# Performance work log

Measured on AMD Instinct MI355X. Metric: run time of the kernel, lower is better.

## Reference

```python
import jax, jax.numpy as jnp
import numpy as np

LOG_CLAMP = -100.0  # torch BCELoss clamps each log term at -100


def setup_inputs() -> dict:
    key = jax.random.key(0)
    k1, k2, k3 = jax.random.split(key, 3)
    B, N, W, H = 256, 32, 1920, 1080
    pred_x = jax.random.uniform(k1, (B, N, W), dtype=jnp.float32)
    pred_y = jax.random.uniform(k2, (B, N, H), dtype=jnp.float32)
    target_ball_position = jax.random.randint(k3, (B, N, 2), 0, 1080, dtype=jnp.int64)
    return {"pred_x": pred_x, "pred_y": pred_y,
            "target_ball_position": target_ball_position}


def _axis_bce(pred, tgt):
    """Per-(b,n) mean BCE against an implicit one-hot target along last axis.

    pred: [B, N, L] probabilities; tgt: [B, N] int indices (already clamped).
    Returns [B, N] losses. Avoids materializing the one-hot:
      mean_i BCE_i = (-log p[t] - sum_{i != t} log(1 - p[i])) / L
    with torch-style clamping of each log term at -100.
    """
    L = pred.shape[-1]
    lp = jnp.maximum(jnp.log(pred), LOG_CLAMP)          # [B,N,L]
    l1p = jnp.maximum(jnp.log1p(-pred), LOG_CLAMP)      # [B,N,L]
    t = tgt[..., None]                                   # [B,N,1]
    lp_t = jnp.take_along_axis(lp, t, axis=-1)[..., 0]   # [B,N]
    l1p_t = jnp.take_along_axis(l1p, t, axis=-1)[..., 0]
    sum_l1p = jnp.sum(l1p, axis=-1)                      # [B,N]
    return (-lp_t - (sum_l1p - l1p_t)) / L


def reference(pred_x, pred_y, target_ball_position):
    W = pred_x.shape[2]
    H = pred_y.shape[2]
    tx = jnp.clip(target_ball_position[..., 0].astype(jnp.int32), 0, W - 1)  # [B,N]
    ty = jnp.clip(target_ball_position[..., 1].astype(jnp.int32), 0, H - 1)
    valid = jnp.logical_not((tx == 0) & (ty == 0))       # [B,N]
    vmask = valid.astype(pred_x.dtype)
    loss_x = _axis_bce(pred_x, tx)                       # [B,N]
    loss_y = _axis_bce(pred_y, ty)
    valid_count = jnp.sum(vmask)
    total_x = jnp.sum(loss_x * vmask)
    total_y = jnp.sum(loss_y * vmask)
    denom = jnp.maximum(valid_count, 1.0)  # if count==0 totals are 0 anyway
    return total_x / denom + total_y / denom
```

## Files before the change

### kernel.cpp

```cpp
#include <hip/hip_runtime.h>

#define WDIM 1920
#define HDIM 1080
#define TPB 256
#define NBLK 2048
#define PAIRS 8192
#define X4 (PAIRS * (WDIM / 4))
#define Y4 (PAIRS * (HDIM / 4))

__device__ __forceinline__ float clog1m(float p) {
    return fmaxf(__log2f(1.f - p) * 0.69314718056f, -100.f);
}
__device__ __forceinline__ float clog(float p) {
    return fmaxf(__log2f(p) * 0.69314718056f, -100.f);
}

__global__ __launch_bounds__(TPB) void bce_main(const float* __restrict__ px,
                                                const float* __restrict__ py,
                                                const int2* __restrict__ tgt,
                                                float* __restrict__ partial_loss,
                                                float* __restrict__ partial_cnt) {
    const int tid = blockIdx.x * TPB + threadIdx.x;
    const int stride = NBLK * TPB;
    const int t = threadIdx.x;
    float acc = 0.f;
    float cnt = 0.f;

    if (tid < PAIRS) {
        int2 t2 = tgt[tid];
        int tx = min(max(t2.x, 0), WDIM - 1);
        int ty = min(max(t2.y, 0), HDIM - 1);
        if (!(tx == 0 && ty == 0)) {
            float pt = px[(size_t)tid * WDIM + tx];
            float qt = py[(size_t)tid * HDIM + ty];
            acc += (clog1m(pt) - clog(pt)) * (1.f / WDIM)
                 + (clog1m(qt) - clog(qt)) * (1.f / HDIM);
            cnt = 1.f;
        }
    }

    const float4* px4 = (const float4*)px;
    const float4* py4 = (const float4*)py;

    for (int i = tid; i < X4; i += stride) {
        float4 v = px4[i];
        int pair = i / 480;
        int2 t2 = tgt[pair];
        int tx = min(max(t2.x, 0), WDIM - 1);
        int ty = min(max(t2.y, 0), HDIM - 1);
        float w = (tx == 0 && ty == 0) ? 0.f : -(1.f / WDIM);
        acc += w * (clog1m(v.x) + clog1m(v.y) + clog1m(v.z) + clog1m(v.w));
    }
    for (int i = tid; i < Y4; i += stride) {
        float4 v = py4[i];
        int pair = i / 270;
        int2 t2 = tgt[pair];
        int tx = min(max(t2.x, 0), WDIM - 1);
        int ty = min(max(t2.y, 0), HDIM - 1);
        float w = (tx == 0 && ty == 0) ? 0.f : -(1.f / HDIM);
        acc += w * (clog1m(v.x) + clog1m(v.y) + clog1m(v.z) + clog1m(v.w));
    }

    #pragma unroll
    for (int o = 32; o > 0; o >>= 1) {
        acc += __shfl_down(acc, o, 64);
        cnt += __shfl_down(cnt, o, 64);
    }
    __shared__ float rs[TPB / 64], rc[TPB / 64];
    if ((t & 63) == 0) { rs[t >> 6] = acc; rc[t >> 6] = cnt; }
    __syncthreads();
    if (t == 0) {
        partial_loss[blockIdx.x] = rs[0] + rs[1] + rs[2] + rs[3];
        partial_cnt[blockIdx.x]  = rc[0] + rc[1] + rc[2] + rc[3];
    }
}

__global__ __launch_bounds__(TPB) void bce_final(const float* __restrict__ pl,
                                                 const float* __restrict__ pc,
                                                 int nblk, float* __restrict__ out) {
    const int t = threadIdx.x;
    float s = 0.f, c = 0.f;
    for (int i = t; i < nblk; i += TPB) { s += pl[i]; c += pc[i]; }
    #pragma unroll
    for (int o = 32; o > 0; o >>= 1) {
        s += __shfl_down(s, o, 64);
        c += __shfl_down(c, o, 64);
    }
    __shared__ float rs[TPB / 64], rc[TPB / 64];
    if ((t & 63) == 0) { rs[t >> 6] = s; rc[t >> 6] = c; }
    __syncthreads();
    if (t == 0) {
        float ts = rs[0] + rs[1] + rs[2] + rs[3];
        float tc = rc[0] + rc[1] + rc[2] + rc[3];
        out[0] = ts / fmaxf(tc, 1.f);
    }
}

extern "C" void kernel_launch(void* const* d_in, const int* in_sizes, int n_in,
                              void* d_out, int out_size, void* d_ws, size_t ws_size,
                              hipStream_t stream) {
    const float* px = (const float*)d_in[0];
    const float* py = (const float*)d_in[1];
    const int2* tgt = (const int2*)d_in[2];
    float* out = (float*)d_out;

    float* pl = (float*)d_ws;
    float* pc = pl + NBLK;

    bce_main<<<dim3(NBLK), dim3(TPB), 0, stream>>>(px, py, tgt, pl, pc);
    bce_final<<<1, TPB, 0, stream>>>(pl, pc, NBLK, out);
}
```

Measured before the change: 118.0 us.

## Give each block four pairs, preload float4s, and fuse four logs into one

Each block now owns four contiguous (b,n) rows instead of grid-striding. The per-row validity weights are computed once into shared memory, which removes the per-element target loads and integer divisions by 480 or 270. All float4 loads for a thread are issued up front into registers so many requests are in flight at once. The sum of four log(1-p) terms becomes one log of their product, cutting transcendental work by four. In exchange the per-element -100 clamp is dropped, so p equal to 1 gives -inf where the reference gives -100.

```diff
diff --git a/kernel.cpp b/kernel.cpp
--- a/kernel.cpp
+++ b/kernel.cpp
@@ -3,16 +3,18 @@
 #define WDIM 1920
 #define HDIM 1080
 #define TPB 256
+#define PPB 4
 #define NBLK 2048
 #define PAIRS 8192
-#define X4 (PAIRS * (WDIM / 4))
-#define Y4 (PAIRS * (HDIM / 4))
+#define XF4 (PPB * WDIM / 4)
+#define YF4 (PPB * HDIM / 4)
+#define LN2 0.69314718056f
 
 __device__ __forceinline__ float clog1m(float p) {
-    return fmaxf(__log2f(1.f - p) * 0.69314718056f, -100.f);
+    return fmaxf(__log2f(1.f - p) * LN2, -100.f);
 }
-__device__ __forceinline__ float clog(float p) {
-    return fmaxf(__log2f(p) * 0.69314718056f, -100.f);
+__device__ __forceinline__ float clogp(float p) {
+    return fmaxf(__log2f(p) * LN2, -100.f);
 }
 
 __global__ __launch_bounds__(TPB) void bce_main(const float* __restrict__ px,
@@ -20,45 +22,67 @@
                                                 const int2* __restrict__ tgt,
                                                 float* __restrict__ partial_loss,
                                                 float* __restrict__ partial_cnt) {
-    const int tid = blockIdx.x * TPB + threadIdx.x;
-    const int stride = NBLK * TPB;
     const int t = threadIdx.x;
-    float acc = 0.f;
-    float cnt = 0.f;
+    const int blk = blockIdx.x;
+    const int tid = blk * TPB + t;
 
+    __shared__ float wx[PPB], wy[PPB];
+    if (t < PPB) {
+        int2 t2 = tgt[blk * PPB + t];
+        int cx = min(max(t2.x, 0), WDIM - 1);
+        int cy = min(max(t2.y, 0), HDIM - 1);
+        float vm = (cx == 0 && cy == 0) ? 0.f : 1.f;
+        wx[t] = vm * (-LN2 / WDIM);
+        wy[t] = vm * (-LN2 / HDIM);
+    }
+
+    float acc = 0.f, cnt = 0.f;
     if (tid < PAIRS) {
         int2 t2 = tgt[tid];
-        int tx = min(max(t2.x, 0), WDIM - 1);
-        int ty = min(max(t2.y, 0), HDIM - 1);
-        if (!(tx == 0 && ty == 0)) {
-            float pt = px[(size_t)tid * WDIM + tx];
-            float qt = py[(size_t)tid * HDIM + ty];
-            acc += (clog1m(pt) - clog(pt)) * (1.f / WDIM)
-                 + (clog1m(qt) - clog(qt)) * (1.f / HDIM);
+        int cx = min(max(t2.x, 0), WDIM - 1);
+        int cy = min(max(t2.y, 0), HDIM - 1);
+        if (!(cx == 0 && cy == 0)) {
+            float pt = px[(size_t)tid * WDIM + cx];
+            float qt = py[(size_t)tid * HDIM + cy];
+            acc += (clog1m(pt) - clogp(pt)) * (1.f / WDIM)
+                 + (clog1m(qt) - clogp(qt)) * (1.f / HDIM);
             cnt = 1.f;
         }
     }
+    __syncthreads();
 
-    const float4* px4 = (const float4*)px;
-    const float4* py4 = (const float4*)py;
+    const float4* bx = (const float4*)px + (size_t)blk * XF4;
+    const float4* by = (const float4*)py + (size_t)blk * YF4;
+    const float4 z4 = make_float4(0.f, 0.f, 0.f, 0.f);
 
-    for (int i = tid; i < X4; i += stride) {
-        float4 v = px4[i];
-        int pair = i / 480;
-        int2 t2 = tgt[pair];
-        int tx = min(max(t2.x, 0), WDIM - 1);
-        int ty = min(max(t2.y, 0), HDIM - 1);
-        float w = (tx == 0 && ty == 0) ? 0.f : -(1.f / WDIM);
-        acc += w * (clog1m(v.x) + clog1m(v.y) + clog1m(v.z) + clog1m(v.w));
+    float4 vx[8];
+    #pragma unroll
+    for (int j = 0; j < 8; ++j) {
+        int idx = t + j * TPB;
+        vx[j] = (j < 7 || t < XF4 - 7 * TPB) ? bx[idx] : z4;
     }
-    for (int i = tid; i < Y4; i += stride) {
-        float4 v = py4[i];
-        int pair = i / 270;
-        int2 t2 = tgt[pair];
-        int tx = min(max(t2.x, 0), WDIM - 1);
-        int ty = min(max(t2.y, 0), HDIM - 1);
-        float w = (tx == 0 && ty == 0) ? 0.f : -(1.f / HDIM);
-        acc += w * (clog1m(v.x) + clog1m(v.y) + clog1m(v.z) + clog1m(v.w));
+    #pragma unroll
+    for (int j = 0; j < 8; ++j) {
+        int idx = t + j * TPB;
+        int pl = idx / 480;
+        float4 v = vx[j];
+        float q = (1.f - v.x) * (1.f - v.y) * (1.f - v.z) * (1.f - v.w);
+        acc += wx[pl] * __log2f(q);
+    }
+
+    float4 vy[5];
+    #pragma unroll
+    for (int j = 0; j < 5; ++j) {
+        int idx = t + j * TPB;
+        vy[j] = (j < 4 || t < YF4 - 4 * TPB) ? by[idx] : z4;
+    }
+    #pragma unroll
+    for (int j = 0; j < 5; ++j) {
+        int idx = t + j * TPB;
+        int pl = idx / 270;
+        float4 v = vy[j];
+        float q = (1.f - v.x) * (1.f - v.y) * (1.f - v.z) * (1.f - v.w);
+        acc += wy[pl] * __log2f(q);
     }
 
     #pragma unroll
@@ -70,8 +94,8 @@
     if ((t & 63) == 0) { rs[t >> 6] = acc; rc[t >> 6] = cnt; }
     __syncthreads();
     if (t == 0) {
-        partial_loss[blockIdx.x] = rs[0] + rs[1] + rs[2] + rs[3];
-        partial_cnt[blockIdx.x]  = rc[0] + rc[1] + rc[2] + rc[3];
+        partial_loss[blk] = rs[0] + rs[1] + rs[2] + rs[3];
+        partial_cnt[blk]  = rc[0] + rc[1] + rc[2] + rc[3];
     }
 }
 
```

Measured after the change: 115.8 us. Within noise of the previous version (-1.9%).
